# Optimization experiments

Hardware: AMD Instinct MI355X
Metric: run time of the kernel (lower is better)

The kernel has to match this reference:

```python
import jax, jax.numpy as jnp
import numpy as np

BATCH = 8
N_CLASSES = 3            # including background
PRE_NMS_LIMIT = 6000
NMS_THRESH = 0.5
SCALE = 512.0
WINDOW = (0.0, 0.0, 512.0, 512.0)   # y1, x1, y2, x2
STD_DEV = np.array([0.1, 0.1, 0.2, 0.2], np.float32)
GROUP_OFFSET = 4096.0    # > image extent; separates (batch, class) groups in NMS

_RATIOS = np.array([0.5, 1.0, 2.0])
_LEVELS = [((128, 128), 4, 8.0), ((64, 64), 8, 16.0), ((32, 32), 16, 32.0), ((16, 16), 32, 64.0)]


def _gen_anchors():
    # faithful port of generate_pyramid_anchors / generate_anchors (anchor_stride=1)
    out = []
    for (fy, fx), stride, scale in _LEVELS:
        s, r = np.meshgrid(np.array([scale]), _RATIOS)
        s, r = s.flatten(), r.flatten()
        heights = s / np.sqrt(r)
        widths = s * np.sqrt(r)
        sy = np.arange(fy) * stride
        sx = np.arange(fx) * stride
        sx, sy = np.meshgrid(sx, sy)
        bw, bcx = np.meshgrid(widths, sx)
        bh, bcy = np.meshgrid(heights, sy)
        centers = np.stack([bcy, bcx], axis=2).reshape(-1, 2)
        sizes = np.stack([bh, bw], axis=2).reshape(-1, 2)
        out.append(np.concatenate([centers - 0.5 * sizes, centers + 0.5 * sizes], axis=1))
    return np.concatenate(out, axis=0).astype(np.float32)  # (65280, 4) yxyx


def setup_inputs() -> dict:
    key = jax.random.key(0)
    k1, k2 = jax.random.split(key)
    anchors = jnp.asarray(_gen_anchors())
    n_anchors = anchors.shape[0]
    n_prop = BATCH * n_anchors
    logits = jax.random.normal(k1, (n_prop, N_CLASSES), jnp.float32)
    probs = jax.nn.softmax(logits, axis=-1)
    deltas = jax.random.normal(k2, (n_prop, 4), jnp.float32)
    batch_ixs = jnp.repeat(jnp.arange(BATCH, dtype=jnp.int64), n_anchors)
    return {"probs": probs, "deltas": deltas, "anchors": anchors, "batch_ixs": batch_ixs}


def _apply_box_deltas_2d(boxes, deltas):
    # boxes: (K,4) yxyx (normalized); deltas: (K,4) dy,dx,dh,dw
    h = boxes[:, 2] - boxes[:, 0]
    w = boxes[:, 3] - boxes[:, 1]
    cy = boxes[:, 0] + 0.5 * h + deltas[:, 0] * h
    cx = boxes[:, 1] + 0.5 * w + deltas[:, 1] * w
    h = h * jnp.exp(deltas[:, 2])
    w = w * jnp.exp(deltas[:, 3])
    y1 = cy - 0.5 * h
    x1 = cx - 0.5 * w
    return jnp.stack([y1, x1, y1 + h, x1 + w], axis=1)


def _nms_keep(boxes, thresh):
    # boxes (K,4), already sorted by score descending; returns bool keep mask.
    y1, x1, y2, x2 = boxes[:, 0], boxes[:, 1], boxes[:, 2], boxes[:, 3]
    areas = (y2 - y1 + 1.0) * (x2 - x1 + 1.0)
    ih = jnp.clip(jnp.minimum(y2[:, None], y2[None, :]) - jnp.maximum(y1[:, None], y1[None, :]) + 1.0, 0.0)
    iw = jnp.clip(jnp.minimum(x2[:, None], x2[None, :]) - jnp.maximum(x1[:, None], x1[None, :]) + 1.0, 0.0)
    inter = ih * iw
    iou = inter / (areas[:, None] + areas[None, :] - inter)  # (K,K)
    K = boxes.shape[0]
    idx = jnp.arange(K)

    def body(i, keep):
        sup = (iou[i] >= thresh) & (idx > i) & keep[i]
        return keep & ~sup

    return jax.lax.fori_loop(0, K, body, jnp.ones((K,), bool))


def reference(probs, deltas, anchors, batch_ixs):
    n_anchors = anchors.shape[0]
    n_fg = probs.shape[1] - 1
    # trim to top pre_nms_limit foreground scores (flat over proposals x fg classes)
    fg = probs[:, 1:].reshape(-1)
    scores, flat_ix = jax.lax.top_k(fg, PRE_NMS_LIMIT)  # sorted descending
    prop_ix = flat_ix // n_fg
    class_ids = flat_ix % n_fg + 1
    b = batch_ixs[prop_ix]
    a = anchors[prop_ix % n_anchors]        # anchors tiled per batch element
    d = deltas[prop_ix] * jnp.asarray(STD_DEV)
    rois = _apply_box_deltas_2d(a / SCALE, d) * SCALE
    lo = jnp.array([WINDOW[0], WINDOW[1], WINDOW[0], WINDOW[1]], rois.dtype)
    hi = jnp.array([WINDOW[2], WINDOW[3], WINDOW[2], WINDOW[3]], rois.dtype)
    rois = jnp.clip(rois, lo, hi)
    # batched per-class NMS: offset boxes so different (batch, class) groups never overlap
    group = (b * (n_fg + 1) + class_ids).astype(rois.dtype) * GROUP_OFFSET
    keep = _nms_keep(rois + group[:, None], NMS_THRESH)
    detections = jnp.concatenate(
        [rois, scores[:, None], keep.astype(rois.dtype)[:, None]], axis=1)  # (K, 6)
    return detections, class_ids, b
```

## Files before the change

kernel.cpp:

```cpp
#include <hip/hip_runtime.h>
#include <math.h>

typedef unsigned int u32;
typedef unsigned short u16;
typedef unsigned long long u64;

#define PRE_NMS 6000
#define NBLK    94
#define KMAX    640
#define MSTRIDE 11
#define FINEB   8192
#define LOWB    8064
#define TOTB    (FINEB + LOWB)
#define NHB     16
#define CANDMAX 16384
#define SLICES  8
#define NGRP    24
#define CBLK    256
#define CBUF    512
#define FLOOR_BITS 0x3F000000u

#define CTR_OFF   0
#define RANKS_OFF 256
#define PART_OFF  65792
#define CAND_OFF  1106176
#define BOXR_OFF  1237248
#define GBITS_OFF 1333504

__global__ __launch_bounds__(1024) void hist_kernel(const float4* __restrict__ probs4,
                                                    u32* __restrict__ partials, int n_prop) {
    __shared__ u32 hf[FINEB];
    __shared__ u32 hl[2][LOWB];
    int t = threadIdx.x;
    for (int i = t; i < FINEB; i += 1024) hf[i] = 0u;
    for (int i = t; i < 2 * LOWB; i += 1024) ((u32*)hl)[i] = 0u;
    __syncthreads();
    u32* l = hl[(t >> 6) & 1];
    int nq = n_prop >> 2;
    int idx = blockIdx.x * 1024 + t;
    int stride = gridDim.x * 1024;
    for (int q = idx; q < nq; q += stride) {
        float4 a = probs4[3 * q + 0];
        float4 b = probs4[3 * q + 1];
        float4 c = probs4[3 * q + 2];
        float vs[8] = {a.y, a.z, b.x, b.y, b.w, c.x, c.z, c.w};
        #pragma unroll
        for (int e = 0; e < 8; ++e) {
            u32 bits = __float_as_uint(vs[e]);
            if (bits >= FLOOR_BITS) {
                u32 fb = (bits - FLOOR_BITS) >> 10; if (fb >= FINEB) fb = FINEB - 1;
                atomicAdd(&hf[fb], 1u);
            } else {
                atomicAdd(&l[bits >> 17], 1u);
            }
        }
    }
    __syncthreads();
    u32* outp = partials + blockIdx.x * TOTB;
    for (int b = t; b < FINEB; b += 1024) outp[b] = hf[b];
    for (int b = t; b < LOWB; b += 1024) outp[FINEB + b] = hl[0][b] + hl[1][b];
}

__global__ __launch_bounds__(1024) void pivot_kernel(const u32* __restrict__ partials,
                                                     u32* __restrict__ ctr,
                                                     u32* __restrict__ ranks,
                                                     u32* __restrict__ gbits) {
    __shared__ u32 fh[FINEB];
    __shared__ u32 sd[1024];
    int t = threadIdx.x;
    for (int i = t; i < CANDMAX; i += 1024) ranks[i] = 0u;
    for (int i = t; i < NGRP * 192; i += 1024) gbits[i] = 0u;
    if (t == 0) ctr[0] = 0u;
    for (int b = t; b < FINEB; b += 1024) {
        u32 s = 0;
        #pragma unroll
        for (int k = 0; k < NHB; ++k) s += partials[k * TOTB + b];
        fh[b] = s;
    }
    __syncthreads();
    int hi = FINEB - 1 - 8 * t;
    u32 L = 0;
    #pragma unroll
    for (int e = 0; e < 8; ++e) L += fh[hi - e];
    sd[t] = L;
    __syncthreads();
    for (int off = 1; off < 1024; off <<= 1) {
        u32 x = (t >= off) ? sd[t - off] : 0u;
        __syncthreads();
        sd[t] += x;
        __syncthreads();
    }
    u32 incl = sd[t], excl = incl - L;
    u32 fineTotal = sd[1023];
    if (excl < (u32)PRE_NMS && incl >= (u32)PRE_NMS) {
        u32 run = excl;
        #pragma unroll
        for (int e = 0; e < 8; ++e) {
            u32 c = fh[hi - e];
            if (run < (u32)PRE_NMS && run + c >= (u32)PRE_NMS)
                ctr[1] = FLOOR_BITS + ((u32)(hi - e) << 10);
            run += c;
        }
    }
    if (fineTotal >= (u32)PRE_NMS) return;

    u32 rem = (u32)PRE_NMS - fineTotal;
    __syncthreads();
    for (int b = t; b < FINEB; b += 1024) {
        u32 s = 0;
        if (b < LOWB) {
            #pragma unroll
            for (int k = 0; k < NHB; ++k) s += partials[k * TOTB + FINEB + b];
        }
        fh[b] = s;
    }
    __syncthreads();
    L = 0;
    #pragma unroll
    for (int e = 0; e < 8; ++e) L += fh[hi - e];
    sd[t] = L;
    __syncthreads();
    for (int off = 1; off < 1024; off <<= 1) {
        u32 x = (t >= off) ? sd[t - off] : 0u;
        __syncthreads();
        sd[t] += x;
        __syncthreads();
    }
    incl = sd[t]; excl = incl - L;
    if (excl < rem && incl >= rem) {
        u32 run = excl;
        #pragma unroll
        for (int e = 0; e < 8; ++e) {
            u32 c = fh[hi - e];
            if (run < rem && run + c >= rem)
                ctr[1] = ((u32)(hi - e)) << 17;
            run += c;
        }
    }
}

__global__ __launch_bounds__(256) void compact_kernel(const float4* __restrict__ probs4,
                                                      u32* ctr, u64* __restrict__ cand,
                                                      int n_prop) {
    __shared__ u64 sloc[CBUF];
    __shared__ u32 scnt, sbase;
    int t = threadIdx.x;
    if (t == 0) scnt = 0u;
    __syncthreads();
    u32 pivot = ctr[1];
    int nq = n_prop >> 2;
    int idx = blockIdx.x * 256 + t;
    int stride = gridDim.x * 256;
    for (int q = idx; q < nq; q += stride) {
        float4 a = probs4[3 * q + 0];
        float4 b = probs4[3 * q + 1];
        float4 c = probs4[3 * q + 2];
        float vs[8] = {a.y, a.z, b.x, b.y, b.w, c.x, c.z, c.w};
        #pragma unroll
        for (int e = 0; e < 8; ++e) {
            u32 bits = __float_as_uint(vs[e]);
            if (bits >= pivot) {
                u32 lp = atomicAdd(&scnt, 1u);
                u32 i = (u32)(8 * q + e);
                if (lp < (u32)CBUF) sloc[lp] = ((u64)bits << 32) | (u64)(~i);
            }
        }
    }
    __syncthreads();
    u32 cnt = scnt; if (cnt > (u32)CBUF) cnt = (u32)CBUF;
    if (t == 0) sbase = atomicAdd(&ctr[0], cnt);
    __syncthreads();
    u32 base = sbase;
    for (u32 j = t; j < cnt; j += 256) {
        u32 pos = base + j;
        if (pos < (u32)CANDMAX) cand[pos] = sloc[j];
    }
}

__global__ __launch_bounds__(256) void rank_kernel(const u64* __restrict__ cand,
                                                   const u32* __restrict__ ctr,
                                                   u32* __restrict__ ranks) {
    __shared__ u64 tile[256];
    int t = threadIdx.x;
    u32 M = ctr[0]; if (M > (u32)CANDMAX) M = (u32)CANDMAX;
    int kb = blockIdx.y;
    if ((u32)(kb * 256) >= M) return;
    int i = kb * 256 + t;
    u64 key = (i < (int)M) ? cand[i] : 0ull;
    u32 Ls = (M + SLICES - 1) / SLICES;
    u32 s0 = blockIdx.x * Ls;
    u32 s1 = s0 + Ls; if (s1 > M) s1 = M;
    int cnt = 0;
    for (u32 base = s0; base < s1; base += 256) {
        u32 idx = base + t;
        tile[t] = (idx < s1) ? cand[idx] : 0ull;
        __syncthreads();
        #pragma unroll 8
        for (int q = 0; q < 256; ++q) cnt += (tile[q] > key) ? 1 : 0;
        __syncthreads();
    }
    if (i < (int)M && cnt > 0) atomicAdd(&ranks[i], (u32)cnt);
}

__global__ __launch_bounds__(256) void decode_kernel(const u64* __restrict__ cand,
                                                     const u32* __restrict__ ranks,
                                                     const u32* __restrict__ ctr,
                                                     const float4* __restrict__ deltas4,
                                                     const float4* __restrict__ anchors4,
                                                     float4* __restrict__ boxr,
                                                     u32* __restrict__ gbits,
                                                     float* __restrict__ out,
                                                     int n_anch) {
    u32 i = blockIdx.x * 256 + threadIdx.x;
    u32 M = ctr[0]; if (M > (u32)CANDMAX) M = (u32)CANDMAX;
    if (i >= M) return;
    u32 r = ranks[i];
    if (r >= (u32)PRE_NMS) return;
    u64 key = cand[i];
    u32 bits = (u32)(key >> 32);
    u32 flat = ~((u32)key);
    int p = (int)(flat >> 1);
    int cls = (int)(flat & 1u) + 1;
    int b = p / n_anch;
    int g = b * 3 + cls;
    int aidx = p - b * n_anch;
    float score = __uint_as_float(bits);
    float4 a = anchors4[aidx];
    float4 d = deltas4[p];
    float d0 = d.x * 0.1f, d1 = d.y * 0.1f, d2 = d.z * 0.2f, d3 = d.w * 0.2f;
    float y1 = a.x * (1.0f / 512.0f), x1 = a.y * (1.0f / 512.0f);
    float y2 = a.z * (1.0f / 512.0f), x2 = a.w * (1.0f / 512.0f);
    float h = y2 - y1, w = x2 - x1;
    float cy = y1 + 0.5f * h + d0 * h;
    float cx = x1 + 0.5f * w + d1 * w;
    h = h * expf(d2);
    w = w * expf(d3);
    float ry1 = (cy - 0.5f * h) * 512.0f;
    float rx1 = (cx - 0.5f * w) * 512.0f;
    float ry2 = (cy - 0.5f * h + h) * 512.0f;
    float rx2 = (cx - 0.5f * w + w) * 512.0f;
    ry1 = fminf(fmaxf(ry1, 0.0f), 512.0f);
    rx1 = fminf(fmaxf(rx1, 0.0f), 512.0f);
    ry2 = fminf(fmaxf(ry2, 0.0f), 512.0f);
    rx2 = fminf(fmaxf(rx2, 0.0f), 512.0f);
    out[r * 6 + 0] = ry1;
    out[r * 6 + 1] = rx1;
    out[r * 6 + 2] = ry2;
    out[r * 6 + 3] = rx2;
    out[r * 6 + 4] = score;
    out[r * 6 + 5] = 1.0f;
    out[PRE_NMS * 6 + r] = (float)cls;
    out[PRE_NMS * 7 + r] = (float)b;
    boxr[r] = make_float4(ry1, rx1, ry2, rx2);
    atomicOr(&gbits[g * 192 + (r >> 5)], 1u << (r & 31));
}

__global__ __launch_bounds__(512) void nms_kernel(const u32* __restrict__ gbits,
                                                  const float4* __restrict__ boxr,
                                                  float* __restrict__ out) {
    __shared__ u64 maskm[KMAX * MSTRIDE + 64];
    __shared__ float4 sbox[KMAX];
    __shared__ float sarea[KMAX];
    __shared__ int bpre[96];
    __shared__ u16 grank[KMAX];
    __shared__ int sK;
    int g = blockIdx.x, t = threadIdx.x, lane = t & 63, wv = t >> 6;
    const u32* rb32 = gbits + g * 192;

    if (t < 64) {
        u64 w0 = (u64)rb32[2 * lane] | ((u64)rb32[2 * lane + 1] << 32);
        u64 w1 = (lane < NBLK - 64)
                 ? ((u64)rb32[128 + 2 * lane] | ((u64)rb32[129 + 2 * lane] << 32)) : 0ull;
        int c0 = (int)__popcll(w0), c1 = (int)__popcll(w1);
        int i0 = c0, i1 = c1;
        #pragma unroll
        for (int off = 1; off < 64; off <<= 1) {
            int a = __shfl_up(i0, off); if (lane >= off) i0 += a;
            int b = __shfl_up(i1, off); if (lane >= off) i1 += b;
        }
        int tot0 = __shfl(i0, 63), tot1 = __shfl(i1, 63);
        bpre[lane] = i0 - c0;
        if (lane < 32) bpre[64 + lane] = tot0 + ((lane < NBLK - 64) ? (i1 - c1) : 0);
        if (lane == 0) sK = tot0 + tot1;
    }
    __syncthreads();
    int K = sK;
    if (K == 0) return;
    int Kc = (K < KMAX) ? K : KMAX;
    int W = (Kc + 63) >> 6;

    for (int m = t; m < KMAX; m += 512) {
        sbox[m] = make_float4(-3e30f, -3e30f, -3e30f, -3e30f);
        sarea[m] = 3e38f;
    }
    for (int m = t; m < KMAX * MSTRIDE + 64; m += 512) maskm[m] = 0ull;
    __syncthreads();

    for (int blk = wv; blk < NBLK; blk += 8) {
        u64 wmask = (u64)rb32[2 * blk] | ((u64)rb32[2 * blk + 1] << 32);
        if ((wmask >> lane) & 1ull) {
            int pos = bpre[blk] + (int)__popcll(wmask & ((1ull << lane) - 1ull));
            if (pos < KMAX) grank[pos] = (u16)((blk << 6) | lane);
        }
    }
    __syncthreads();

    for (int m = t; m < Kc; m += 512) {
        float4 bb = boxr[grank[m]];
        sbox[m] = bb;
        sarea[m] = (bb.z - bb.x + 1.0f) * (bb.w - bb.y + 1.0f);
    }
    __syncthreads();

    int unit = 0;
    for (int c = 0; c < W; ++c) {
        int j0 = c << 6;
        for (int rb0 = 0; rb0 < Kc && rb0 < j0 + 63; rb0 += 64, ++unit) {
            if ((unit & 7) != wv) continue;
            int r = rb0 + lane;
            float4 rb = sbox[r];
            float ra = sarea[r];
            u64 word = 0ull;
            #pragma unroll 8
            for (int q = 0; q < 64; ++q) {
                int cc = j0 + q;
                float4 cb = sbox[cc];
                float ih = fminf(rb.z, cb.z) - fmaxf(rb.x, cb.x) + 1.0f;
                float iw = fminf(rb.w, cb.w) - fmaxf(rb.y, cb.y) + 1.0f;
                ih = fmaxf(ih, 0.0f); iw = fmaxf(iw, 0.0f);
                bool o = (3.0f * ih * iw >= ra + sarea[cc]) && (cc > r);
                if (o) word |= (1ull << q);
            }
            maskm[r * MSTRIDE + c] = word;
        }
    }
    __syncthreads();

    if (t >= 64) return;
    u64 remv = 0ull;
    for (int w = 0; w < W; ++w) {
        int r0 = w << 6;
        int rend = Kc - r0; if (rend > 64) rend = 64;
        u64 curw = __shfl(remv, w);
        u64 kb = 0ull;
        for (int b0 = 0; b0 < rend; b0 += 8) {
            int n = rend - b0; if (n > 8) n = 8;
            u64 mrow[8], dg[8];
            #pragma unroll
            for (int j = 0; j < 8; ++j) {
                int rr = r0 + b0 + ((j < n) ? j : 0);
                mrow[j] = maskm[rr * MSTRIDE + lane];
                dg[j]   = maskm[rr * MSTRIDE + w];
            }
            #pragma unroll
            for (int j = 0; j < 8; ++j) {
                if (j < n) {
                    int b = b0 + j;
                    u64 km = ((curw >> b) & 1ull) ? 0ull : ~0ull;
                    curw |= dg[j] & km;
                    remv |= mrow[j] & km;
                    kb |= km & (1ull << b);
                }
            }
        }
        if (lane < rend)
            out[(int)grank[r0 + lane] * 6 + 5] = ((kb >> lane) & 1ull) ? 1.0f : 0.0f;
    }
}

extern "C" void kernel_launch(void* const* d_in, const int* in_sizes, int n_in,
                              void* d_out, int out_size, void* d_ws, size_t ws_size,
                              hipStream_t stream) {
    const float*  probs    = (const float*)d_in[0];
    const float4* deltas4  = (const float4*)d_in[1];
    const float4* anchors4 = (const float4*)d_in[2];
    int n_prop = in_sizes[1] / 4;
    int n_anch = in_sizes[2] / 4;

    char* ws = (char*)d_ws;
    u32* ctr      = (u32*)(ws + CTR_OFF);
    u32* ranks    = (u32*)(ws + RANKS_OFF);
    u32* partials = (u32*)(ws + PART_OFF);
    u64* cand     = (u64*)(ws + CAND_OFF);
    float4* boxr  = (float4*)(ws + BOXR_OFF);
    u32* gbits    = (u32*)(ws + GBITS_OFF);
    float* out    = (float*)d_out;

    hist_kernel<<<NHB, 1024, 0, stream>>>((const float4*)probs, partials, n_prop);
    pivot_kernel<<<1, 1024, 0, stream>>>(partials, ctr, ranks, gbits);
    compact_kernel<<<CBLK, 256, 0, stream>>>((const float4*)probs, ctr, cand, n_prop);
    rank_kernel<<<dim3(SLICES, 64), 256, 0, stream>>>(cand, ctr, ranks);
    decode_kernel<<<CANDMAX / 256, 256, 0, stream>>>(cand, ranks, ctr, deltas4, anchors4,
                                                     boxr, gbits, out, n_anch);
    nms_kernel<<<NGRP, 512, 0, stream>>>(gbits, boxr, out);
}
```

Baseline: 160.1 us.

## Split NMS into prep, parallel mask, and greedy kernels across many blocks

The single 24-block NMS kernel becomes three kernels. A prep kernel gathers each group's boxes into global memory. A mask kernel then computes the IoU bitmask tiles using one 64-thread block per (tile, group) and broadcasts column boxes with shuffles. A greedy kernel loads the mask into shared memory and runs the sequential suppression. The aim is to spread the mask computation over many more CUs than 24 blocks could use, at the cost of two extra launches and a global-memory round trip for boxes and masks.

```diff
diff --git a/kernel.cpp b/kernel.cpp
--- a/kernel.cpp
+++ b/kernel.cpp
@@ -9,6 +9,8 @@
 #define NBLK    94
 #define KMAX    640
 #define MSTRIDE 11
+#define MAXW    10
+#define MTILE   (MAXW * MAXW)
 #define FINEB   8192
 #define LOWB    8064
 #define TOTB    (FINEB + LOWB)
@@ -20,12 +22,17 @@
 #define CBUF    512
 #define FLOOR_BITS 0x3F000000u
 
-#define CTR_OFF   0
-#define RANKS_OFF 256
-#define PART_OFF  65792
-#define CAND_OFF  1106176
-#define BOXR_OFF  1237248
-#define GBITS_OFF 1333504
+#define CTR_OFF    0
+#define RANKS_OFF  256
+#define PART_OFF   65792
+#define CAND_OFF   1106176
+#define BOXR_OFF   1237248
+#define GBITS_OFF  1333504
+#define KG_OFF     1351936
+#define GRANKG_OFF 1352192
+#define BOXG_OFF   1413632
+#define AREAG_OFF  1659392
+#define MASKG_OFF  1720832
 
 __global__ __launch_bounds__(1024) void hist_kernel(const float4* __restrict__ probs4,
                                                     u32* __restrict__ partials, int n_prop) {
@@ -255,14 +262,14 @@
     atomicOr(&gbits[g * 192 + (r >> 5)], 1u << (r & 31));
 }
 
-__global__ __launch_bounds__(512) void nms_kernel(const u32* __restrict__ gbits,
-                                                  const float4* __restrict__ boxr,
-                                                  float* __restrict__ out) {
-    __shared__ u64 maskm[KMAX * MSTRIDE + 64];
-    __shared__ float4 sbox[KMAX];
-    __shared__ float sarea[KMAX];
+__global__ __launch_bounds__(512) void prep_kernel(const u32* __restrict__ gbits,
+                                                   const float4* __restrict__ boxr,
+                                                   u32* __restrict__ kg,
+                                                   u32* __restrict__ grankg,
+                                                   float4* __restrict__ boxg,
+                                                   float* __restrict__ areag) {
     __shared__ int bpre[96];
-    __shared__ u16 grank[KMAX];
+    __shared__ u16 grankS[KMAX];
     __shared__ int sK;
     int g = blockIdx.x, t = threadIdx.x, lane = t & 63, wv = t >> 6;
     const u32* rb32 = gbits + g * 192;
@@ -281,59 +288,95 @@
         int tot0 = __shfl(i0, 63), tot1 = __shfl(i1, 63);
         bpre[lane] = i0 - c0;
         if (lane < 32) bpre[64 + lane] = tot0 + ((lane < NBLK - 64) ? (i1 - c1) : 0);
-        if (lane == 0) sK = tot0 + tot1;
+        if (lane == 0) { sK = tot0 + tot1; kg[g] = (u32)(tot0 + tot1); }
     }
     __syncthreads();
     int K = sK;
     if (K == 0) return;
     int Kc = (K < KMAX) ? K : KMAX;
-    int W = (Kc + 63) >> 6;
-
-    for (int m = t; m < KMAX; m += 512) {
-        sbox[m] = make_float4(-3e30f, -3e30f, -3e30f, -3e30f);
-        sarea[m] = 3e38f;
-    }
-    for (int m = t; m < KMAX * MSTRIDE + 64; m += 512) maskm[m] = 0ull;
-    __syncthreads();
 
     for (int blk = wv; blk < NBLK; blk += 8) {
         u64 wmask = (u64)rb32[2 * blk] | ((u64)rb32[2 * blk + 1] << 32);
         if ((wmask >> lane) & 1ull) {
             int pos = bpre[blk] + (int)__popcll(wmask & ((1ull << lane) - 1ull));
-            if (pos < KMAX) grank[pos] = (u16)((blk << 6) | lane);
-        }
-    }
-    __syncthreads();
-
-    for (int m = t; m < Kc; m += 512) {
-        float4 bb = boxr[grank[m]];
-        sbox[m] = bb;
-        sarea[m] = (bb.z - bb.x + 1.0f) * (bb.w - bb.y + 1.0f);
-    }
-    __syncthreads();
-
-    int unit = 0;
-    for (int c = 0; c < W; ++c) {
-        int j0 = c << 6;
-        for (int rb0 = 0; rb0 < Kc && rb0 < j0 + 63; rb0 += 64, ++unit) {
-            if ((unit & 7) != wv) continue;
-            int r = rb0 + lane;
-            float4 rb = sbox[r];
-            float ra = sarea[r];
-            u64 word = 0ull;
-            #pragma unroll 8
-            for (int q = 0; q < 64; ++q) {
-                int cc = j0 + q;
-                float4 cb = sbox[cc];
-                float ih = fminf(rb.z, cb.z) - fmaxf(rb.x, cb.x) + 1.0f;
-                float iw = fminf(rb.w, cb.w) - fmaxf(rb.y, cb.y) + 1.0f;
-                ih = fmaxf(ih, 0.0f); iw = fmaxf(iw, 0.0f);
-                bool o = (3.0f * ih * iw >= ra + sarea[cc]) && (cc > r);
-                if (o) word |= (1ull << q);
-            }
-            maskm[r * MSTRIDE + c] = word;
-        }
-    }
+            if (pos < KMAX) grankS[pos] = (u16)((blk << 6) | lane);
+        }
+    }
+    __syncthreads();
+
+    float4* bg = boxg + g * KMAX;
+    float*  ag = areag + g * KMAX;
+    u32*    gr = grankg + g * KMAX;
+    for (int m = t; m < KMAX; m += 512) {
+        if (m < Kc) {
+            int r = grankS[m];
+            float4 bb = boxr[r];
+            bg[m] = bb;
+            ag[m] = (bb.z - bb.x + 1.0f) * (bb.w - bb.y + 1.0f);
+            gr[m] = (u32)r;
+        } else {
+            bg[m] = make_float4(-3e30f, -3e30f, -3e30f, -3e30f);
+            ag[m] = 3e38f;
+        }
+    }
+}
+
+__global__ __launch_bounds__(64) void mask_kernel(const u32* __restrict__ kg,
+                                                  const float4* __restrict__ boxg,
+                                                  const float* __restrict__ areag,
+                                                  u64* __restrict__ maskg) {
+    int g = blockIdx.y;
+    u32 K = kg[g];
+    if (K == 0u) return;
+    int Kc = (K < (u32)KMAX) ? (int)K : KMAX;
+    int W = (Kc + 63) >> 6;
+    int u = blockIdx.x;
+    int c = u / MAXW, rbk = u % MAXW;
+    if (c >= W || rbk >= W) return;
+    int lane = threadIdx.x;
+    int r = rbk * 64 + lane;
+    u64* mg = maskg + (size_t)g * (KMAX * MSTRIDE);
+    if (rbk > c) { mg[r * MSTRIDE + c] = 0ull; return; }
+    int j0 = c << 6;
+    const float4* bg = boxg + g * KMAX;
+    const float*  ag = areag + g * KMAX;
+    float4 rb = bg[r];
+    float  ra = ag[r];
+    float4 cb = bg[j0 + lane];
+    float  ca = ag[j0 + lane];
+    u64 word = 0ull;
+    #pragma unroll 8
+    for (int q = 0; q < 64; ++q) {
+        float cbx = __shfl(cb.x, q);
+        float cby = __shfl(cb.y, q);
+        float cbz = __shfl(cb.z, q);
+        float cbw = __shfl(cb.w, q);
+        float cav = __shfl(ca, q);
+        float ih = fminf(rb.z, cbz) - fmaxf(rb.x, cbx) + 1.0f;
+        float iw = fminf(rb.w, cbw) - fmaxf(rb.y, cby) + 1.0f;
+        ih = fmaxf(ih, 0.0f); iw = fmaxf(iw, 0.0f);
+        bool o = (3.0f * ih * iw >= ra + cav) && ((j0 + q) > r);
+        if (o) word |= (1ull << q);
+    }
+    mg[r * MSTRIDE + c] = word;
+}
+
+__global__ __launch_bounds__(512) void greedy_kernel(const u32* __restrict__ kg,
+                                                     const u32* __restrict__ grankg,
+                                                     const u64* __restrict__ maskg,
+                                                     float* __restrict__ out) {
+    __shared__ u64 maskm[KMAX * MSTRIDE + 64];
+    __shared__ u16 grank[KMAX];
+    int g = blockIdx.x, t = threadIdx.x, lane = t & 63;
+    u32 K = kg[g];
+    if (K == 0u) return;
+    int Kc = (K < (u32)KMAX) ? (int)K : KMAX;
+    int W = (Kc + 63) >> 6;
+    const u64* mg = maskg + (size_t)g * (KMAX * MSTRIDE);
+    int nw = Kc * MSTRIDE;
+    for (int m = t; m < nw; m += 512) maskm[m] = mg[m];
+    for (int m = nw + t; m < nw + 64; m += 512) maskm[m] = 0ull;
+    for (int m = t; m < Kc; m += 512) grank[m] = (u16)grankg[g * KMAX + m];
     __syncthreads();
 
     if (t >= 64) return;
@@ -384,6 +427,11 @@
     u64* cand     = (u64*)(ws + CAND_OFF);
     float4* boxr  = (float4*)(ws + BOXR_OFF);
     u32* gbits    = (u32*)(ws + GBITS_OFF);
+    u32* kg       = (u32*)(ws + KG_OFF);
+    u32* grankg   = (u32*)(ws + GRANKG_OFF);
+    float4* boxg  = (float4*)(ws + BOXG_OFF);
+    float* areag  = (float*)(ws + AREAG_OFF);
+    u64* maskg    = (u64*)(ws + MASKG_OFF);
     float* out    = (float*)d_out;
 
     hist_kernel<<<NHB, 1024, 0, stream>>>((const float4*)probs, partials, n_prop);
@@ -392,5 +440,7 @@
     rank_kernel<<<dim3(SLICES, 64), 256, 0, stream>>>(cand, ctr, ranks);
     decode_kernel<<<CANDMAX / 256, 256, 0, stream>>>(cand, ranks, ctr, deltas4, anchors4,
                                                      boxr, gbits, out, n_anch);
-    nms_kernel<<<NGRP, 512, 0, stream>>>(gbits, boxr, out);
-}
+    prep_kernel<<<NGRP, 512, 0, stream>>>(gbits, boxr, kg, grankg, boxg, areag);
+    mask_kernel<<<dim3(MTILE, NGRP), 64, 0, stream>>>(kg, boxg, areag, maskg);
+    greedy_kernel<<<NGRP, 512, 0, stream>>>(kg, grankg, maskg, out);
+}
```

New measurement: 153.5 us. 4.1% less time.
